# Performance work log

Measured on AMD Instinct MI355X. Metric: run time of the kernel, lower is better.

Reference implementation:

```python
import jax, jax.numpy as jnp
import numpy as np

EPS = 1e-5

def batchnorm2d(x, gamma, beta):
    # training-mode BN over (N, T, V) per channel; x: [N, C, T, V]
    mean = jnp.mean(x, axis=(0, 2, 3), keepdims=True)
    var = jnp.var(x, axis=(0, 2, 3), keepdims=True)
    xhat = (x - mean) * jax.lax.rsqrt(var + EPS)
    return xhat * gamma[None, :, None, None] + beta[None, :, None, None]

def temporal_shift(x, theta, stride):
    # learnable per-channel temporal shift with linear interpolation, zero pad
    # x: [N, C, T, V], theta: [C]
    N, C, T, V = x.shape
    T_out = T // stride
    t = jnp.arange(T_out, dtype=theta.dtype)
    pos = t[None, :] * stride + theta[:, None]          # [C, T_out]
    i0 = jnp.floor(pos).astype(jnp.int32)
    frac = (pos - i0.astype(theta.dtype))[None, :, :, None]  # [1,C,T_out,1]
    cidx = jnp.arange(C)[:, None]                        # [C, 1]

    def gather(idx):
        valid = (idx >= 0) & (idx < T)
        g = x[:, cidx, jnp.clip(idx, 0, T - 1), :]       # [N, C, T_out, V]
        return jnp.where(valid[None, :, :, None], g, 0.0)

    return gather(i0) * (1.0 - frac) + gather(i0 + 1) * frac

def setup_inputs() -> dict:
    key = jax.random.key(0)
    k = jax.random.split(key, 6)
    N, Cin, Cout, T, V = 64, 256, 256, 64, 25
    x = jax.random.normal(k[0], (N, Cin, T, V), dtype=jnp.float32)
    # kaiming normal fan_out for 1x1 conv: std = sqrt(2 / (Cout*1*1))
    conv_w = jax.random.normal(k[1], (Cout, Cin), dtype=jnp.float32) * np.float32(np.sqrt(2.0 / Cout))
    conv_b = jnp.zeros((Cout,), dtype=jnp.float32)
    bn1_g = jnp.ones((Cin,), dtype=jnp.float32)
    bn1_b = jnp.zeros((Cin,), dtype=jnp.float32)
    bn2_g = jnp.ones((Cin,), dtype=jnp.float32)   # bn_init(bn2, 1)
    bn2_b = jnp.zeros((Cin,), dtype=jnp.float32)
    theta_in = jax.random.uniform(k[2], (Cin,), jnp.float32, -1.0, 1.0)
    theta_out = jax.random.uniform(k[3], (Cout,), jnp.float32, -1.0, 1.0)
    return {"x": x, "conv_w": conv_w, "conv_b": conv_b,
            "bn1_g": bn1_g, "bn1_b": bn1_b, "bn2_g": bn2_g, "bn2_b": bn2_b,
            "theta_in": theta_in, "theta_out": theta_out}

def reference(x, conv_w, conv_b, bn1_g, bn1_b, bn2_g, bn2_b, theta_in, theta_out):
    stride = 1
    h = batchnorm2d(x, bn1_g, bn1_b)
    h = temporal_shift(h, theta_in, 1)
    h = jnp.einsum('nctv,oc->notv', h, conv_w) + conv_b[None, :, None, None]
    h = jax.nn.relu(h)
    h = temporal_shift(h, theta_out, stride)
    h = batchnorm2d(h, bn2_g, bn2_b)
    return h
```

## Files before the change

### kernel.cpp

```cpp
#include <hip/hip_runtime.h>


#define EPSV 1e-5f
constexpr int Nn = 64, Cc = 256, Tt = 64, Vv = 25;
constexpr int TV = Tt * Vv;
constexpr int CTV = Cc * TV;
constexpr float Minv = 1.0f / (Nn * TV);

typedef short short8 __attribute__((ext_vector_type(8)));
typedef float floatx4 __attribute__((ext_vector_type(4)));

__device__ __forceinline__ unsigned short f2bf(float f) {
    unsigned int u = __builtin_bit_cast(unsigned int, f);
    u += 0x7FFFu + ((u >> 16) & 1u);
    return (unsigned short)(u >> 16);
}
__device__ __forceinline__ float bflo(unsigned int w) {
    return __builtin_bit_cast(float, w << 16);
}
__device__ __forceinline__ float bfhi(unsigned int w) {
    return __builtin_bit_cast(float, w & 0xFFFF0000u);
}
__device__ __forceinline__ void unp8v(uint4 u, float* o) {
    o[0] = bflo(u.x); o[1] = bfhi(u.x); o[2] = bflo(u.y); o[3] = bfhi(u.y);
    o[4] = bflo(u.z); o[5] = bfhi(u.z); o[6] = bflo(u.w); o[7] = bfhi(u.w);
}
__device__ __forceinline__ void gload_lds16(const void* g, void* l) {
    __builtin_amdgcn_global_load_lds((const __attribute__((address_space(1))) void*)g,
                                     (__attribute__((address_space(3))) void*)l, 16, 0, 0);
}

__global__ __launch_bounds__(256) void k_stats_shift(const float* __restrict__ x,
                                                     const float* __restrict__ theta,
                                                     float* __restrict__ sacc,
                                                     float* __restrict__ qacc,
                                                     unsigned short* __restrict__ ht) {
    int c0 = blockIdx.x * 64;
    int E0 = blockIdx.y * 200;
    int n  = blockIdx.z;
    int tid = threadIdx.x;
    __shared__ __attribute__((aligned(16))) unsigned short xt[256][68];
    __shared__ int   pd[64];
    __shared__ float pf[64];
    if (tid < 64) {
        float th = theta[c0 + tid];
        float fd = floorf(th);
        pd[tid] = (int)fd;
        pf[tid] = th - fd;
    }
    int lo = E0 - 28; if (lo < 0) lo = 0;
    int hi = E0 + 228; if (hi > 1600) hi = 1600;
    int ldsoff = lo - (E0 - 28);
    int nf4 = (hi - lo) >> 2;
    {
        int cp = tid >> 3, li = tid & 7;
        int ca = 2 * cp;
        const float4* xr0 = (const float4*)(x + (size_t)n * CTV + (size_t)(c0 + ca) * TV + lo);
        const float4* xr1 = xr0 + (TV >> 2);
        float4 v0[8], v1[8];
#pragma unroll
        for (int s = 0; s < 8; ++s) {
            int i = li + s * 8;
            if (i < nf4) { v0[s] = xr0[i]; v1[s] = xr1[i]; }
        }
        float s0 = 0.f, q0 = 0.f, s1 = 0.f, q1 = 0.f;
#pragma unroll
        for (int s = 0; s < 8; ++s) {
            int i = li + s * 8;
            if (i < nf4) {
                int r = ldsoff + i * 4;
#pragma unroll
                for (int k = 0; k < 4; ++k) {
                    float a = ((const float*)&v0[s])[k];
                    float b = ((const float*)&v1[s])[k];
                    if ((unsigned)(r + k - 28) < 200u) {
                        s0 += a; q0 += a * a; s1 += b; q1 += b * b;
                    }
                    unsigned int pk = (unsigned int)f2bf(a) | (((unsigned int)f2bf(b)) << 16);
                    *(unsigned int*)&xt[r + k][ca] = pk;
                }
            }
        }
        for (int off = 4; off; off >>= 1) {
            s0 += __shfl_down(s0, off); q0 += __shfl_down(q0, off);
            s1 += __shfl_down(s1, off); q1 += __shfl_down(q1, off);
        }
        if (li == 0) {
            atomicAdd(&sacc[c0 + ca], s0);     atomicAdd(&qacc[c0 + ca], q0);
            atomicAdd(&sacc[c0 + ca + 1], s1); atomicAdd(&qacc[c0 + ca + 1], q1);
        }
    }
    __syncthreads();
    int cseg = tid & 7, er = tid >> 3;
    int cb = cseg * 8;
    int dk[8]; float fk[8];
#pragma unroll
    for (int k = 0; k < 8; ++k) { dk[k] = pd[cb + k]; fk[k] = pf[cb + k]; }
    for (int it = 0; it < 7; ++it) {
        int tv_l = er + it * 32;
        if (tv_l >= 200) break;
        int e = E0 + tv_l;
        float A8[8], B8[8], C8[8];
        {
            const unsigned short* rA = &xt[tv_l + 3][cb];
            const unsigned short* rB = &xt[tv_l + 28][cb];
            const unsigned short* rC = &xt[tv_l + 53][cb];
            uint2 a0 = *(const uint2*)rA, a1 = *(const uint2*)(rA + 4);
            uint2 b0 = *(const uint2*)rB, b1 = *(const uint2*)(rB + 4);
            uint2 g0 = *(const uint2*)rC, g1 = *(const uint2*)(rC + 4);
            A8[0]=bflo(a0.x); A8[1]=bfhi(a0.x); A8[2]=bflo(a0.y); A8[3]=bfhi(a0.y);
            A8[4]=bflo(a1.x); A8[5]=bfhi(a1.x); A8[6]=bflo(a1.y); A8[7]=bfhi(a1.y);
            B8[0]=bflo(b0.x); B8[1]=bfhi(b0.x); B8[2]=bflo(b0.y); B8[3]=bfhi(b0.y);
            B8[4]=bflo(b1.x); B8[5]=bfhi(b1.x); B8[6]=bflo(b1.y); B8[7]=bfhi(b1.y);
            C8[0]=bflo(g0.x); C8[1]=bfhi(g0.x); C8[2]=bflo(g0.y); C8[3]=bfhi(g0.y);
            C8[4]=bflo(g1.x); C8[5]=bfhi(g1.x); C8[6]=bflo(g1.y); C8[7]=bfhi(g1.y);
        }
        unsigned int w4[4];
#pragma unroll
        for (int k = 0; k < 8; ++k) {
            int d = dk[k]; float f = fk[k];
            float x0 = (d < 0) ? A8[k] : B8[k];
            float x1 = (d < 0) ? B8[k] : C8[k];
            int e0 = e + 25 * d;
            float v0 = ((unsigned)e0 < 1600u) ? x0 : 0.f;
            float v1 = ((unsigned)(e0 + 25) < 1600u) ? x1 : 0.f;
            unsigned short hb = f2bf(v0 + f * (v1 - v0));
            if (k & 1) w4[k >> 1] |= ((unsigned int)hb) << 16;
            else       w4[k >> 1] = hb;
        }
        uint4 st = { w4[0], w4[1], w4[2], w4[3] };
        *(uint4*)(ht + (size_t)(n * 1600 + e) * 256 + c0 + cb) = st;
    }
}

__global__ __launch_bounds__(256) void k_params(const float* __restrict__ w,
                                                const float* __restrict__ bias,
                                                const float* __restrict__ sacc,
                                                const float* __restrict__ qacc,
                                                const float* __restrict__ g,
                                                const float* __restrict__ b,
                                                const float* __restrict__ theta,
                                                unsigned short* __restrict__ wb,
                                                float* __restrict__ b2all,
                                                float* __restrict__ s0v,
                                                float* __restrict__ s63v) {
    int o = blockIdx.x, c = threadIdx.x;
    float mean = sacc[c] * Minv;
    float var  = qacc[c] * Minv - mean * mean;
    float sc = g[c] * rsqrtf(var + EPSV);
    float tc = b[c] - mean * sc;
    float th = theta[c];
    float fd = floorf(th);
    int d = (int)fd;
    float f = th - fd;
    float wv = w[o * 256 + c];
    wb[o * 256 + c] = f2bf(wv * sc);
    float wtc = wv * tc;
    float r0  = (d < 0) ? wtc * (1.f - f) : 0.f;
    float r63 = (d == 0) ? wtc * f : 0.f;
    for (int off = 32; off; off >>= 1) {
        wtc += __shfl_down(wtc, off);
        r0  += __shfl_down(r0, off);
        r63 += __shfl_down(r63, off);
    }
    __shared__ float aux[3][4];
    if ((c & 63) == 0) { int wi = c >> 6; aux[0][wi] = wtc; aux[1][wi] = r0; aux[2][wi] = r63; }
    __syncthreads();
    if (c == 0) {
        b2all[o] = bias[o] + aux[0][0] + aux[0][1] + aux[0][2] + aux[0][3];
        s0v[o]  = aux[1][0] + aux[1][1] + aux[1][2] + aux[1][3];
        s63v[o] = aux[2][0] + aux[2][1] + aux[2][2] + aux[2][3];
    }
}

__global__ __launch_bounds__(256) void k_gemm(const unsigned short* __restrict__ ht,
                                              const unsigned short* __restrict__ wb,
                                              const float* __restrict__ b2all,
                                              const float* __restrict__ s0v,
                                              const float* __restrict__ s63v,
                                              unsigned short* __restrict__ y) {
    int j0 = blockIdx.x * 128;
    int tid = threadIdx.x;
    int w = tid >> 6, lane = tid & 63;
    int quad = lane >> 4, l16 = lane & 15;
    __shared__ __attribute__((aligned(16))) unsigned short smem[24576];
    floatx4 acc[4][8] = {};
    int sg = (lane & 3) ^ ((lane >> 3) & 3);
    const unsigned short* wpA = wb + (size_t)(w * 64 + (lane >> 2)) * 256 + sg * 8;
    const unsigned short* hpB = ht + (size_t)(j0 + w * 32 + (lane >> 2)) * 256 + sg * 8;
    int rg = quad ^ ((l16 >> 1) & 3);

#define STAGE(buf, k0)                                                              \
    {                                                                               \
        unsigned short* Ab_ = smem + (buf) * 12288;                                 \
        unsigned short* Bb_ = Ab_ + 8192;                                           \
        _Pragma("unroll")                                                           \
        for (int a = 0; a < 4; ++a)                                                 \
            gload_lds16(wpA + (size_t)a * 16 * 256 + (k0), Ab_ + (w * 64 + a * 16) * 32); \
        _Pragma("unroll")                                                           \
        for (int b = 0; b < 2; ++b)                                                 \
            gload_lds16(hpB + (size_t)b * 16 * 256 + (k0), Bb_ + (w * 32 + b * 16) * 32); \
    }
#define COMPUTE(buf)                                                                \
    {                                                                               \
        const unsigned short* Ab_ = smem + (buf) * 12288;                           \
        const unsigned short* Bb_ = Ab_ + 8192;                                     \
        short8 af[4];                                                               \
        _Pragma("unroll")                                                           \
        for (int m = 0; m < 4; ++m)                                                 \
            af[m] = *(const short8*)&Ab_[(w * 64 + m * 16 + l16) * 32 + rg * 8];    \
        _Pragma("unroll")                                                           \
        for (int jt = 0; jt < 8; ++jt) {                                            \
            short8 bfr = *(const short8*)&Bb_[(jt * 16 + l16) * 32 + rg * 8];       \
            _Pragma("unroll")                                                       \
            for (int m = 0; m < 4; ++m)                                             \
                acc[m][jt] = __builtin_amdgcn_mfma_f32_16x16x32_bf16(af[m], bfr, acc[m][jt], 0, 0, 0); \
        }                                                                           \
    }

    STAGE(0, 0)
    asm volatile("s_waitcnt vmcnt(0)" ::: "memory");
    __builtin_amdgcn_s_barrier();
#pragma unroll
    for (int t = 0; t < 8; t += 2) {
        if (t + 1 < 8) STAGE(1, (t + 1) * 32)
        COMPUTE(0)
        asm volatile("s_waitcnt vmcnt(0)" ::: "memory");
        __builtin_amdgcn_s_barrier();
        if (t + 2 < 8) STAGE(0, (t + 2) * 32)
        COMPUTE(1)
        asm volatile("s_waitcnt vmcnt(0)" ::: "memory");
        __builtin_amdgcn_s_barrier();
    }
#undef STAGE
#undef COMPUTE

    unsigned short* Cl = smem;
    int li = tid & 15, orow = tid >> 4;
#pragma unroll
    for (int p = 0; p < 2; ++p) {
        if ((w >> 1) == p) {
            int rowbase = (w & 1) * 64;
#pragma unroll
            for (int m = 0; m < 4; ++m) {
                int ob = p * 128 + (w & 1) * 64 + m * 16 + quad * 4;
#pragma unroll
                for (int r = 0; r < 4; ++r) {
                    int o = ob + r;
                    float bb = b2all[o], e0 = s0v[o], e63 = s63v[o];
                    int lrow = rowbase + m * 16 + quad * 4 + r;
#pragma unroll
                    for (int jt = 0; jt < 8; ++jt) {
                        int jj = j0 + jt * 16;
                        int nn = jj / 1600;
                        int tvb = jj - nn * 1600 + l16;
                        float bia = bb - (tvb < 25 ? e0 : 0.f) - (tvb >= 1575 ? e63 : 0.f);
                        float v = acc[m][jt][r] + bia;
                        v = v > 0.f ? v : 0.f;
                        Cl[lrow * 136 + jt * 16 + l16] = f2bf(v);
                    }
                }
            }
        }
        __syncthreads();
#pragma unroll
        for (int pass = 0; pass < 8; ++pass) {
            int ol = orow + pass * 16;
            uint4 vv = *(const uint4*)&Cl[ol * 136 + li * 8];
            int o = p * 128 + ol;
            int j = j0 + li * 8;
            int nn = j / 1600;
            int tv = j - nn * 1600;
            *(uint4*)(y + (size_t)nn * CTV + (size_t)o * TV + tv) = vv;
        }
        if (p == 0) __syncthreads();
    }
}

__global__ __launch_bounds__(256) void k_bn2_stats(const unsigned short* __restrict__ y,
                                                   float* __restrict__ acc7) {
    int o = blockIdx.y, ng = blockIdx.x, tid = threadIdx.x;
    float S = 0.f, Q = 0.f, P = 0.f, Y0 = 0.f, Q0 = 0.f, Y63 = 0.f, Q63 = 0.f;
    if (tid < 200) {
        int e = tid * 8;
        int eB = e + 24; if (eB > 1592) eB = 1592;
        int eC = e + 32; if (eC > 1592) eC = 1592;
        const unsigned short* base0 = y + (size_t)(ng * 8) * CTV + (size_t)o * TV;
        uint4 ua = *(const uint4*)(base0 + e);
        uint4 ub = *(const uint4*)(base0 + eB);
        uint4 uc = *(const uint4*)(base0 + eC);
        for (int nn = 0; nn < 8; ++nn) {
            uint4 na, nb, nc;
            if (nn < 7) {
                const unsigned short* row = base0 + (size_t)(nn + 1) * CTV;
                na = *(const uint4*)(row + e);
                nb = *(const uint4*)(row + eB);
                nc = *(const uint4*)(row + eC);
            }
            float a[8], b[8], c[8];
            unp8v(ua, a); unp8v(ub, b); unp8v(uc, c);
#pragma unroll
            for (int k = 0; k < 8; ++k) {
                float v = a[k];
                S += v; Q += v * v;
                float vn = (k < 7) ? b[k + 1] : c[0];
                if (e + k < 1575) P += v * vn;
            }
            if (e < 32) {
#pragma unroll
                for (int k = 0; k < 8; ++k)
                    if (e + k < 25) { Y0 += a[k]; Q0 += a[k] * a[k]; }
            }
            if (e >= 1568) {
#pragma unroll
                for (int k = 0; k < 8; ++k)
                    if (e + k >= 1575) { Y63 += a[k]; Q63 += a[k] * a[k]; }
            }
            ua = na; ub = nb; uc = nc;
        }
    }
    for (int off = 32; off; off >>= 1) {
        S += __shfl_down(S, off); Q += __shfl_down(Q, off); P += __shfl_down(P, off);
        Y0 += __shfl_down(Y0, off); Q0 += __shfl_down(Q0, off);
        Y63 += __shfl_down(Y63, off); Q63 += __shfl_down(Q63, off);
    }
    if ((tid & 63) == 0) {
        atomicAdd(&acc7[o], S);           atomicAdd(&acc7[256 + o], Q);
        atomicAdd(&acc7[512 + o], P);     atomicAdd(&acc7[768 + o], Y0);
        atomicAdd(&acc7[1024 + o], Q0);   atomicAdd(&acc7[1280 + o], Y63);
        atomicAdd(&acc7[1536 + o], Q63);
    }
}

__global__ __launch_bounds__(256) void k_bn2_apply(const unsigned short* __restrict__ y,
                                                   const float* __restrict__ theta,
                                                   const float* __restrict__ acc7,
                                                   const float* __restrict__ g,
                                                   const float* __restrict__ b,
                                                   float* __restrict__ out) {
    int o = blockIdx.y, n = blockIdx.x, tid = threadIdx.x;
    float th = theta[o];
    float fd = floorf(th);
    int d = (int)fd;
    float f = th - fd;
    float S = acc7[o], Q = acc7[256 + o], P = acc7[512 + o];
    float Y0 = acc7[768 + o], Q0 = acc7[1024 + o], Y63 = acc7[1280 + o], Q63 = acc7[1536 + o];
    float omf = 1.f - f;
    float sz, qz;
    if (d < 0) { sz = S - omf * Y63; qz = omf * omf * (Q - Q63) + f * f * Q + 2.f * f * omf * P; }
    else       { sz = S - f * Y0;    qz = omf * omf * Q + f * f * (Q - Q0) + 2.f * f * omf * P; }
    float mean = sz * Minv;
    float var = qz * Minv - mean * mean;
    float sc = g[o] * rsqrtf(var + EPSV);
    float tc = b[o] - mean * sc;
    if (tid >= 200) return;
    int e = tid * 8;
    const unsigned short* row = y + (size_t)n * CTV + (size_t)o * TV;
    float a0[8], a1[8];
    if (d < 0) {
        int eA = e - 32; if (eA < 0) eA = 0;
        int eB = e - 24; if (eB < 0) eB = 0;
        float A[8], B[8], M[8];
        unp8v(*(const uint4*)(row + eA), A);
        unp8v(*(const uint4*)(row + eB), B);
        unp8v(*(const uint4*)(row + e), M);
        a0[0] = (e >= 25) ? A[7] : 0.f;
#pragma unroll
        for (int k = 1; k < 8; ++k) a0[k] = (e + k >= 25) ? B[k - 1] : 0.f;
#pragma unroll
        for (int k = 0; k < 8; ++k) a1[k] = M[k];
    } else {
        int eB = e + 24; if (eB > 1592) eB = 1592;
        int eC = e + 32; if (eC > 1592) eC = 1592;
        float M[8], B[8], C[8];
        unp8v(*(const uint4*)(row + e), M);
        unp8v(*(const uint4*)(row + eB), B);
        unp8v(*(const uint4*)(row + eC), C);
#pragma unroll
        for (int k = 0; k < 8; ++k) a0[k] = M[k];
#pragma unroll
        for (int k = 0; k < 7; ++k) a1[k] = (e + k < 1575) ? B[k + 1] : 0.f;
        a1[7] = (e + 7 < 1575) ? C[0] : 0.f;
    }
    float4 r0, r1;
#pragma unroll
    for (int k = 0; k < 4; ++k) {
        ((float*)&r0)[k] = (omf * a0[k] + f * a1[k]) * sc + tc;
        ((float*)&r1)[k] = (omf * a0[k + 4] + f * a1[k + 4]) * sc + tc;
    }
    float* op = out + (size_t)n * CTV + (size_t)o * TV + e;
    *(float4*)op = r0;
    *(float4*)(op + 4) = r1;
}

extern "C" void kernel_launch(void* const* d_in, const int* in_sizes, int n_in,
                              void* d_out, int out_size, void* d_ws, size_t ws_size,
                              hipStream_t stream) {
    const float* x      = (const float*)d_in[0];
    const float* conv_w = (const float*)d_in[1];
    const float* conv_b = (const float*)d_in[2];
    const float* bn1_g  = (const float*)d_in[3];
    const float* bn1_b  = (const float*)d_in[4];
    const float* bn2_g  = (const float*)d_in[5];
    const float* bn2_b  = (const float*)d_in[6];
    const float* th_in  = (const float*)d_in[7];
    const float* th_out = (const float*)d_in[8];
    float* out = (float*)d_out;

    char* ws = (char*)d_ws;
    unsigned short* ht = (unsigned short*)ws;
    unsigned short* yy = (unsigned short*)(ws + 52428800);
    unsigned short* wb = (unsigned short*)(ws + 104857600);
    float* sacc1 = (float*)(ws + 104988672);
    float* qacc1 = sacc1 + 256;
    float* acc7  = qacc1 + 256;
    float* b2all = acc7 + 7 * 256;
    float* s0v   = b2all + 256;
    float* s63v  = s0v + 256;

    hipMemsetAsync((void*)sacc1, 0, 9 * 256 * sizeof(float), stream);
    hipLaunchKernelGGL(k_stats_shift, dim3(4, 8, 64), dim3(256), 0, stream,
                       x, th_in, sacc1, qacc1, ht);
    hipLaunchKernelGGL(k_params, dim3(256), dim3(256), 0, stream,
                       conv_w, conv_b, sacc1, qacc1, bn1_g, bn1_b, th_in,
                       wb, b2all, s0v, s63v);
    hipLaunchKernelGGL(k_gemm, dim3(800), dim3(256), 0, stream,
                       ht, wb, b2all, s0v, s63v, yy);
    hipLaunchKernelGGL(k_bn2_stats, dim3(8, 256), dim3(256), 0, stream, yy, acc7);
    hipLaunchKernelGGL(k_bn2_apply, dim3(64, 256), dim3(256), 0, stream,
                       yy, th_out, acc7, bn2_g, bn2_b, out);
}
```

Before: 339.6 us.

## Triple-buffer GEMM K-loop, set MFMA priority, and prefetch stats loads

The GEMM kernel moves from a double-buffered to a triple-buffered LDS pipeline, using partial vmcnt waits so the next stage's loads stay in flight during compute. It also raises wave priority around the MFMA loop and adds a launch-bounds occupancy hint. In the stats/shift kernel, loads become a one-ahead software prefetch instead of loading all eight float4 pairs up front, and the transposed LDS row stride is padded from 68 to 70. The extra LDS per block and the occupancy hint may change register allocation and occupancy.

```diff
diff --git a/kernel.cpp b/kernel.cpp
--- a/kernel.cpp
+++ b/kernel.cpp
@@ -39,7 +39,7 @@
     int E0 = blockIdx.y * 200;
     int n  = blockIdx.z;
     int tid = threadIdx.x;
-    __shared__ __attribute__((aligned(16))) unsigned short xt[256][68];
+    __shared__ __attribute__((aligned(16))) unsigned short xt[256][70];
     __shared__ int   pd[64];
     __shared__ float pf[64];
     if (tid < 64) {
@@ -57,22 +57,20 @@
         int ca = 2 * cp;
         const float4* xr0 = (const float4*)(x + (size_t)n * CTV + (size_t)(c0 + ca) * TV + lo);
         const float4* xr1 = xr0 + (TV >> 2);
-        float4 v0[8], v1[8];
+        float s0 = 0.f, q0 = 0.f, s1 = 0.f, q1 = 0.f;
+        float4 acur = xr0[li], bcur = xr1[li];
 #pragma unroll
         for (int s = 0; s < 8; ++s) {
             int i = li + s * 8;
-            if (i < nf4) { v0[s] = xr0[i]; v1[s] = xr1[i]; }
-        }
-        float s0 = 0.f, q0 = 0.f, s1 = 0.f, q1 = 0.f;
-#pragma unroll
-        for (int s = 0; s < 8; ++s) {
-            int i = li + s * 8;
+            int inx = i + 8;
+            float4 anxt, bnxt;
+            if (inx < nf4) { anxt = xr0[inx]; bnxt = xr1[inx]; }
             if (i < nf4) {
                 int r = ldsoff + i * 4;
 #pragma unroll
                 for (int k = 0; k < 4; ++k) {
-                    float a = ((const float*)&v0[s])[k];
-                    float b = ((const float*)&v1[s])[k];
+                    float a = ((const float*)&acur)[k];
+                    float b = ((const float*)&bcur)[k];
                     if ((unsigned)(r + k - 28) < 200u) {
                         s0 += a; q0 += a * a; s1 += b; q1 += b * b;
                     }
@@ -80,6 +78,7 @@
                     *(unsigned int*)&xt[r + k][ca] = pk;
                 }
             }
+            acur = anxt; bcur = bnxt;
         }
         for (int off = 4; off; off >>= 1) {
             s0 += __shfl_down(s0, off); q0 += __shfl_down(q0, off);
@@ -173,17 +172,17 @@
     }
 }
 
-__global__ __launch_bounds__(256) void k_gemm(const unsigned short* __restrict__ ht,
-                                              const unsigned short* __restrict__ wb,
-                                              const float* __restrict__ b2all,
-                                              const float* __restrict__ s0v,
-                                              const float* __restrict__ s63v,
-                                              unsigned short* __restrict__ y) {
+__global__ __launch_bounds__(256, 2) void k_gemm(const unsigned short* __restrict__ ht,
+                                                 const unsigned short* __restrict__ wb,
+                                                 const float* __restrict__ b2all,
+                                                 const float* __restrict__ s0v,
+                                                 const float* __restrict__ s63v,
+                                                 unsigned short* __restrict__ y) {
     int j0 = blockIdx.x * 128;
     int tid = threadIdx.x;
     int w = tid >> 6, lane = tid & 63;
     int quad = lane >> 4, l16 = lane & 15;
-    __shared__ __attribute__((aligned(16))) unsigned short smem[24576];
+    __shared__ __attribute__((aligned(16))) unsigned short smem[36864];
     floatx4 acc[4][8] = {};
     int sg = (lane & 3) ^ ((lane >> 3) & 3);
     const unsigned short* wpA = wb + (size_t)(w * 64 + (lane >> 2)) * 256 + sg * 8;
@@ -209,6 +208,7 @@
         _Pragma("unroll")                                                           \
         for (int m = 0; m < 4; ++m)                                                 \
             af[m] = *(const short8*)&Ab_[(w * 64 + m * 16 + l16) * 32 + rg * 8];    \
+        __builtin_amdgcn_s_setprio(1);                                              \
         _Pragma("unroll")                                                           \
         for (int jt = 0; jt < 8; ++jt) {                                            \
             short8 bfr = *(const short8*)&Bb_[(jt * 16 + l16) * 32 + rg * 8];       \
@@ -216,25 +216,41 @@
             for (int m = 0; m < 4; ++m)                                             \
                 acc[m][jt] = __builtin_amdgcn_mfma_f32_16x16x32_bf16(af[m], bfr, acc[m][jt], 0, 0, 0); \
         }                                                                           \
-    }
+        __builtin_amdgcn_s_setprio(0);                                              \
+    }
+#define WAITVM(n) asm volatile("s_waitcnt vmcnt(" #n ")" ::: "memory")
+#define BAR() __builtin_amdgcn_s_barrier()
 
     STAGE(0, 0)
-    asm volatile("s_waitcnt vmcnt(0)" ::: "memory");
-    __builtin_amdgcn_s_barrier();
-#pragma unroll
-    for (int t = 0; t < 8; t += 2) {
-        if (t + 1 < 8) STAGE(1, (t + 1) * 32)
-        COMPUTE(0)
-        asm volatile("s_waitcnt vmcnt(0)" ::: "memory");
-        __builtin_amdgcn_s_barrier();
-        if (t + 2 < 8) STAGE(0, (t + 2) * 32)
-        COMPUTE(1)
-        asm volatile("s_waitcnt vmcnt(0)" ::: "memory");
-        __builtin_amdgcn_s_barrier();
-    }
+    STAGE(1, 32)
+    WAITVM(6); BAR();
+    STAGE(2, 64)
+    COMPUTE(0)
+    WAITVM(6); BAR();
+    STAGE(0, 96)
+    COMPUTE(1)
+    WAITVM(6); BAR();
+    STAGE(1, 128)
+    COMPUTE(2)
+    WAITVM(6); BAR();
+    STAGE(2, 160)
+    COMPUTE(0)
+    WAITVM(6); BAR();
+    STAGE(0, 192)
+    COMPUTE(1)
+    WAITVM(6); BAR();
+    STAGE(1, 224)
+    COMPUTE(2)
+    WAITVM(6); BAR();
+    COMPUTE(0)
+    WAITVM(0); BAR();
+    COMPUTE(1)
 #undef STAGE
 #undef COMPUTE
-
+#undef WAITVM
+#undef BAR
+
+    __syncthreads();
     unsigned short* Cl = smem;
     int li = tid & 15, orow = tid >> 4;
 #pragma unroll
```

Result: slower. 347.1 us (+2.2%).
